# Optimization experiments

Measured on AMD Instinct MI355X. Metric: run time of the kernel, lower is better.

The kernel has to match this reference:

```python
import jax, jax.numpy as jnp
import numpy as np

EMB = 768
HEADS = 12
HEAD_DIM = EMB // HEADS
SCALE = HEAD_DIM ** -0.5


def setup_inputs() -> dict:
    key = jax.random.key(0)
    kq, kk, kv, kw = jax.random.split(key, 4)
    B, H, N, D = 2, HEADS, 2048, HEAD_DIM
    queries = jax.random.normal(kq, (B, H, N, D), dtype=jnp.float32)
    keys = jax.random.normal(kk, (B, H, N, D), dtype=jnp.float32)
    values = jax.random.normal(kv, (B, H, N, D), dtype=jnp.float32)
    proj_w = jax.random.normal(kw, (EMB, EMB), dtype=jnp.float32) * (EMB ** -0.5)
    proj_b = jnp.zeros((EMB,), dtype=jnp.float32)
    return {"queries": queries, "keys": keys, "values": values,
            "proj_w": proj_w, "proj_b": proj_b}


def reference(queries, keys, values, proj_w, proj_b):
    # energy: [b, h, n, n] -- full quadratic score matrix, as in the original
    energy = jnp.einsum('bhij,bhkj->bhik', queries, keys) * SCALE
    att = jax.nn.softmax(energy, axis=-1)  # att_drop_p=0.0 -> identity
    out = jnp.einsum('bhij,bhjk->bhik', att, values)  # [b, h, n, d]
    b, h, n, d = out.shape
    out = jnp.transpose(out, (0, 2, 1, 3)).reshape(b, n, h * d)  # 'b h n d -> b n (h d)'
    # nn.Linear: x @ W^T + b (projection dropout is inference identity)
    return out @ proj_w.T + proj_b
```

## Files before the change

### kernel.cpp

```cpp
#include <hip/hip_runtime.h>
#include <cstdint>

typedef short bf16x8 __attribute__((ext_vector_type(8)));
typedef float f32x4 __attribute__((ext_vector_type(4)));
typedef uint16_t u16x4 __attribute__((ext_vector_type(4)));

#define MFMA_16x16x32(a, b, c) __builtin_amdgcn_mfma_f32_16x16x32_bf16((a), (b), (c), 0, 0, 0)

static constexpr int BATCH = 2;
static constexpr int HEADS = 12;
static constexpr int NCTX  = 2048;
static constexpr int DH    = 64;
static constexpr int EMB   = 768;

static constexpr float QSCALE = 0.125f * 1.44269504088896340736f;

__device__ __forceinline__ uint16_t f2bf(float x) {
    uint32_t u = __float_as_uint(x);
    u += 0x7FFFu + ((u >> 16) & 1u);
    return (uint16_t)(u >> 16);
}
__device__ __forceinline__ uint32_t cvt_pk_bf16(float lo, float hi) {
    uint32_t r;
    asm("v_cvt_pk_bf16_f32 %0, %1, %2" : "=v"(r) : "v"(lo), "v"(hi));
    return r;
}

__global__ void k_cvt2(const float* __restrict__ a, uint16_t* __restrict__ da, int n4a,
                       const float* __restrict__ b2, uint16_t* __restrict__ db, int n4b) {
    int i = blockIdx.x * blockDim.x + threadIdx.x;
    const float* src; uint16_t* dst; int j;
    if (i < n4a) { src = a; dst = da; j = i; }
    else {
        j = i - n4a;
        if (j >= n4b) return;
        src = b2; dst = db;
    }
    float4 v = reinterpret_cast<const float4*>(src)[j];
    u16x4 hv = {f2bf(v.x), f2bf(v.y), f2bf(v.z), f2bf(v.w)};
    reinterpret_cast<u16x4*>(dst)[j] = hv;
}

__global__ __launch_bounds__(256) void k_vt(const float* __restrict__ v,
                                            uint16_t* __restrict__ vt) {
    const int bh = blockIdx.y;
    const int n0 = blockIdx.x * 64;
    const int t  = threadIdx.x;
    __shared__ uint16_t tileT[64][72];

    const int r  = t >> 2;
    const int cc = (t & 3) * 16;
    const float* vp = v + ((size_t)bh * NCTX + n0 + r) * DH + cc;
#pragma unroll
    for (int u = 0; u < 4; ++u) {
        float4 x = reinterpret_cast<const float4*>(vp)[u];
        tileT[cc + 4 * u + 0][r] = f2bf(x.x);
        tileT[cc + 4 * u + 1][r] = f2bf(x.y);
        tileT[cc + 4 * u + 2][r] = f2bf(x.z);
        tileT[cc + 4 * u + 3][r] = f2bf(x.w);
    }
    __syncthreads();

    const int l2 = t & 63;
    const int s0 = t >> 6;
    const int gg = l2 >> 4;
    const int c2 = l2 & 15;
    uint16_t* vb = vt + ((size_t)bh * 32 + (n0 >> 6)) * 8 * 512;
#pragma unroll
    for (int u = 0; u < 2; ++u) {
        const int slot = s0 + 4 * u;
        const int f = slot >> 1, h = slot & 1;
        bf16x8 x = *reinterpret_cast<const bf16x8*>(&tileT[f * 16 + c2][h * 32 + 8 * gg]);
        *reinterpret_cast<bf16x8*>(vb + (size_t)slot * 512 + l2 * 8) = x;
    }
}

__global__ __launch_bounds__(256) void k_attn(
        const float* __restrict__ q, const uint16_t* __restrict__ kb,
        const uint16_t* __restrict__ vf, uint16_t* __restrict__ xb) {
    const int bh = blockIdx.y;
    const int b  = bh / HEADS;
    const int h  = bh % HEADS;
    const int tid = threadIdx.x;
    const int w = tid >> 6;
    const int l = tid & 63;
    const int g = l >> 4;
    const int c = l & 15;

    __shared__ uint16_t K_s[2][64][72];
    __shared__ uint16_t P_s[4][16][72];

    const int q0 = blockIdx.x * 64 + w * 16;

    bf16x8 qa[2];
    {
        const float* qp = q + ((size_t)bh * NCTX + q0 + c) * DH + 8 * g;
#pragma unroll
        for (int kf = 0; kf < 2; ++kf) {
            float4 x0 = *reinterpret_cast<const float4*>(qp + kf * 32);
            float4 x1 = *reinterpret_cast<const float4*>(qp + kf * 32 + 4);
            bf16x8 f;
            f[0] = (short)f2bf(x0.x * QSCALE); f[1] = (short)f2bf(x0.y * QSCALE);
            f[2] = (short)f2bf(x0.z * QSCALE); f[3] = (short)f2bf(x0.w * QSCALE);
            f[4] = (short)f2bf(x1.x * QSCALE); f[5] = (short)f2bf(x1.y * QSCALE);
            f[6] = (short)f2bf(x1.z * QSCALE); f[7] = (short)f2bf(x1.w * QSCALE);
            qa[kf] = f;
        }
    }

    f32x4 zero = {0.f, 0.f, 0.f, 0.f};
    f32x4 o[4] = {zero, zero, zero, zero};
    float m = -1e30f;
    float lsum = 0.f;

    const int srow = tid >> 3;
    const int sch  = tid & 7;

    const uint16_t* kb_b = kb + (size_t)bh * NCTX * DH + srow * DH + sch * 8;
    const uint16_t* vf_b = vf + (size_t)bh * 32 * 8 * 512 + (size_t)l * 8;

    {
        bf16x8 a0 = *reinterpret_cast<const bf16x8*>(kb_b);
        bf16x8 a1 = *reinterpret_cast<const bf16x8*>(kb_b + 32 * DH);
        *reinterpret_cast<bf16x8*>(&K_s[0][srow][sch * 8])      = a0;
        *reinterpret_cast<bf16x8*>(&K_s[0][srow + 32][sch * 8]) = a1;
    }
    __syncthreads();

    for (int t = 0; t < NCTX / 64; ++t) {
        const int cur = t & 1;
        const int nxt = cur ^ 1;

        bf16x8 nk0, nk1;
        const bool pf = (t + 1) < NCTX / 64;
        if (pf) {
            const size_t ko = (size_t)(t + 1) * 64 * DH;
            nk0 = *reinterpret_cast<const bf16x8*>(kb_b + ko);
            nk1 = *reinterpret_cast<const bf16x8*>(kb_b + ko + 32 * DH);
        }

        bf16x8 vr[8];
#pragma unroll
        for (int s = 0; s < 8; ++s)
            vr[s] = *reinterpret_cast<const bf16x8*>(vf_b + ((size_t)t * 8 + s) * 512);

        f32x4 s[4] = {zero, zero, zero, zero};
        __builtin_amdgcn_s_setprio(1);
#pragma unroll
        for (int nf = 0; nf < 4; ++nf) {
#pragma unroll
            for (int kf = 0; kf < 2; ++kf) {
                bf16x8 bhf = *reinterpret_cast<const bf16x8*>(&K_s[cur][nf * 16 + c][kf * 32 + 8 * g]);
                s[nf] = MFMA_16x16x32(bhf, qa[kf], s[nf]);
            }
        }
        __builtin_amdgcn_s_setprio(0);

        float pm0 = fmaxf(fmaxf(s[0][0], s[0][1]), fmaxf(s[0][2], s[0][3]));
        float pm1 = fmaxf(fmaxf(s[1][0], s[1][1]), fmaxf(s[1][2], s[1][3]));
        float pm2 = fmaxf(fmaxf(s[2][0], s[2][1]), fmaxf(s[2][2], s[2][3]));
        float pm3 = fmaxf(fmaxf(s[3][0], s[3][1]), fmaxf(s[3][2], s[3][3]));
        float pmax = fmaxf(fmaxf(pm0, pm1), fmaxf(pm2, pm3));

        if (!__all(pmax <= m + 11.0f)) {
            float smax = fmaxf(pmax, __shfl_xor(pmax, 16));
            smax = fmaxf(smax, __shfl_xor(smax, 32));
            float mnew = fmaxf(m, smax);
            float corr = __builtin_amdgcn_exp2f(m - mnew);
            m = mnew;
            lsum *= corr;
#pragma unroll
            for (int r = 0; r < 4; ++r) {
                float cr = __shfl(corr, 4 * g + r);
#pragma unroll
                for (int f = 0; f < 4; ++f) o[f][r] *= cr;
            }
        }

#pragma unroll
        for (int nf = 0; nf < 4; ++nf) {
            float p0 = __builtin_amdgcn_exp2f(s[nf][0] - m);
            float p1 = __builtin_amdgcn_exp2f(s[nf][1] - m);
            float p2 = __builtin_amdgcn_exp2f(s[nf][2] - m);
            float p3 = __builtin_amdgcn_exp2f(s[nf][3] - m);
            lsum += (p0 + p1) + (p2 + p3);
            uint2 pk;
            pk.x = cvt_pk_bf16(p0, p1);
            pk.y = cvt_pk_bf16(p2, p3);
            *reinterpret_cast<uint2*>(&P_s[w][c][16 * nf + 4 * g]) = pk;
        }

        bf16x8 pa0 = *reinterpret_cast<const bf16x8*>(&P_s[w][c][8 * g]);
        bf16x8 pa1 = *reinterpret_cast<const bf16x8*>(&P_s[w][c][32 + 8 * g]);
        __builtin_amdgcn_s_setprio(1);
#pragma unroll
        for (int f = 0; f < 4; ++f) {
            o[f] = MFMA_16x16x32(pa0, vr[2 * f],     o[f]);
            o[f] = MFMA_16x16x32(pa1, vr[2 * f + 1], o[f]);
        }
        __builtin_amdgcn_s_setprio(0);

        if (pf) {
            *reinterpret_cast<bf16x8*>(&K_s[nxt][srow][sch * 8])      = nk0;
            *reinterpret_cast<bf16x8*>(&K_s[nxt][srow + 32][sch * 8]) = nk1;
        }
        __syncthreads();
    }

    lsum += __shfl_xor(lsum, 16);
    lsum += __shfl_xor(lsum, 32);
    const float linv = 1.0f / lsum;

    const size_t xbase = ((size_t)b * NCTX + q0) * EMB + h * DH;
#pragma unroll
    for (int r = 0; r < 4; ++r) {
        float lr = __shfl(linv, 4 * g + r);
#pragma unroll
        for (int f = 0; f < 4; ++f) {
            float v = o[f][r] * lr;
            size_t addr = xbase + (size_t)(4 * g + r) * EMB + f * 16 + c;
            xb[addr] = f2bf(v);
        }
    }
}

__global__ __launch_bounds__(256) void k_proj(
        const uint16_t* __restrict__ xb, const uint16_t* __restrict__ wb,
        const float* __restrict__ bias, float* __restrict__ out) {
    const int tid = threadIdx.x;
    const int w = tid >> 6;
    const int l = tid & 63;
    const int g = l >> 4;
    const int c = l & 15;
    const int m0 = blockIdx.x * 64 + w * 16;
    const int n0 = blockIdx.y * 64;

    __shared__ uint16_t W_s[64][72];

    f32x4 zero = {0.f, 0.f, 0.f, 0.f};
    f32x4 acc[4] = {zero, zero, zero, zero};

    const int srow = tid >> 2;
    const int sch  = tid & 3;
    constexpr int ROUNDS = EMB / 64;

    const uint16_t* whp = wb + (size_t)(n0 + srow) * EMB + sch * 8;
    const uint16_t* xhp = xb + (size_t)(m0 + c) * EMB + 8 * g;

    bf16x8 w0 = *reinterpret_cast<const bf16x8*>(whp);
    bf16x8 w1 = *reinterpret_cast<const bf16x8*>(whp + 32);
    bf16x8 a0 = *reinterpret_cast<const bf16x8*>(xhp);
    bf16x8 a1 = *reinterpret_cast<const bf16x8*>(xhp + 32);

    for (int rd = 0; rd < ROUNDS; ++rd) {
        __syncthreads();
        *reinterpret_cast<bf16x8*>(&W_s[srow][sch * 8])      = w0;
        *reinterpret_cast<bf16x8*>(&W_s[srow][32 + sch * 8]) = w1;
        __syncthreads();

        const int rn = (rd + 1 < ROUNDS) ? (rd + 1) : (ROUNDS - 1);
        bf16x8 w0n = *reinterpret_cast<const bf16x8*>(whp + (size_t)rn * 64);
        bf16x8 w1n = *reinterpret_cast<const bf16x8*>(whp + (size_t)rn * 64 + 32);
        bf16x8 a0n = *reinterpret_cast<const bf16x8*>(xhp + (size_t)rn * 64);
        bf16x8 a1n = *reinterpret_cast<const bf16x8*>(xhp + (size_t)rn * 64 + 32);

        __builtin_amdgcn_s_setprio(1);
#pragma unroll
        for (int nf = 0; nf < 4; ++nf) {
            bf16x8 b0 = *reinterpret_cast<const bf16x8*>(&W_s[nf * 16 + c][8 * g]);
            bf16x8 b1 = *reinterpret_cast<const bf16x8*>(&W_s[nf * 16 + c][32 + 8 * g]);
            acc[nf] = MFMA_16x16x32(a0, b0, acc[nf]);
            acc[nf] = MFMA_16x16x32(a1, b1, acc[nf]);
        }
        __builtin_amdgcn_s_setprio(0);

        w0 = w0n; w1 = w1n; a0 = a0n; a1 = a1n;
    }

#pragma unroll
    for (int nf = 0; nf < 4; ++nf) {
#pragma unroll
        for (int r = 0; r < 4; ++r) {
            int row = m0 + g * 4 + r;
            int col = n0 + nf * 16 + c;
            out[(size_t)row * EMB + col] = acc[nf][r] + bias[col];
        }
    }
}

extern "C" void kernel_launch(void* const* d_in, const int* in_sizes, int n_in,
                              void* d_out, int out_size, void* d_ws, size_t ws_size,
                              hipStream_t stream) {
    const float* q    = (const float*)d_in[0];
    const float* k    = (const float*)d_in[1];
    const float* v    = (const float*)d_in[2];
    const float* pw   = (const float*)d_in[3];
    const float* pb   = (const float*)d_in[4];
    float* out = (float*)d_out;

    const size_t nqkv = (size_t)BATCH * HEADS * NCTX * DH;
    const size_t nx   = (size_t)BATCH * NCTX * EMB;
    const size_t nw   = (size_t)EMB * EMB;

    uint8_t* ws = (uint8_t*)d_ws;
    uint16_t* kb = (uint16_t*)ws;              ws += nqkv * 2;
    uint16_t* vf = (uint16_t*)ws;              ws += nqkv * 2;
    uint16_t* xb = (uint16_t*)ws;              ws += nx * 2;
    uint16_t* wb = (uint16_t*)ws;              ws += nw * 2;

    const int n4k = (int)(nqkv / 4);
    const int n4w = (int)(nw / 4);
    k_cvt2<<<(n4k + n4w + 255) / 256, 256, 0, stream>>>(k, kb, n4k, pw, wb, n4w);
    k_vt<<<dim3(NCTX / 64, BATCH * HEADS), 256, 0, stream>>>(v, vf);

    k_attn<<<dim3(NCTX / 64, BATCH * HEADS), 256, 0, stream>>>(q, kb, vf, xb);

    k_proj<<<dim3((BATCH * NCTX) / 64, EMB / 64), 256, 0, stream>>>(xb, wb, pb, out);
}
```

Before: 77.59 us.

## Split attention KV range across two blocks and merge partial softmax results

Attention now runs a split-K style grid: each block processes half of the key/value sequence, and a new merge kernel combines the two partial outputs using their stored row max and sum. This doubles the block count from 768 to 1536, aiming for better occupancy and latency hiding across the GPU's compute units. It also drops the double-buffered K shared tile in favour of a single buffer with an extra barrier. In exchange it adds an extra kernel launch, writes and rereads bf16 partial outputs, and rounds to bf16 an extra time.

```diff
diff --git a/kernel.cpp b/kernel.cpp
--- a/kernel.cpp
+++ b/kernel.cpp
@@ -9,6 +9,7 @@
 
 static constexpr int BATCH = 2;
 static constexpr int HEADS = 12;
+static constexpr int BH    = BATCH * HEADS;
 static constexpr int NCTX  = 2048;
 static constexpr int DH    = 64;
 static constexpr int EMB   = 768;
@@ -19,6 +20,9 @@
     uint32_t u = __float_as_uint(x);
     u += 0x7FFFu + ((u >> 16) & 1u);
     return (uint16_t)(u >> 16);
+}
+__device__ __forceinline__ float bf2f(uint16_t h) {
+    return __uint_as_float(((uint32_t)h) << 16);
 }
 __device__ __forceinline__ uint32_t cvt_pk_bf16(float lo, float hi) {
     uint32_t r;
@@ -77,20 +81,21 @@
 
 __global__ __launch_bounds__(256) void k_attn(
         const float* __restrict__ q, const uint16_t* __restrict__ kb,
-        const uint16_t* __restrict__ vf, uint16_t* __restrict__ xb) {
+        const uint16_t* __restrict__ vf, uint16_t* __restrict__ of,
+        float* __restrict__ ml) {
     const int bh = blockIdx.y;
-    const int b  = bh / HEADS;
-    const int h  = bh % HEADS;
+    const int z  = blockIdx.z;
     const int tid = threadIdx.x;
     const int w = tid >> 6;
     const int l = tid & 63;
     const int g = l >> 4;
     const int c = l & 15;
 
-    __shared__ uint16_t K_s[2][64][72];
+    __shared__ uint16_t K_s[64][72];
     __shared__ uint16_t P_s[4][16][72];
 
     const int q0 = blockIdx.x * 64 + w * 16;
+    constexpr int NT = (NCTX / 2) / 64;
 
     bf16x8 qa[2];
     {
@@ -116,23 +121,20 @@
     const int srow = tid >> 3;
     const int sch  = tid & 7;
 
-    const uint16_t* kb_b = kb + (size_t)bh * NCTX * DH + srow * DH + sch * 8;
-    const uint16_t* vf_b = vf + (size_t)bh * 32 * 8 * 512 + (size_t)l * 8;
+    const uint16_t* kb_b = kb + ((size_t)bh * NCTX + z * (NCTX / 2) + srow) * DH + sch * 8;
+    const uint16_t* vf_b = vf + ((size_t)bh * 32 + z * NT) * 8 * 512 + (size_t)l * 8;
 
     {
         bf16x8 a0 = *reinterpret_cast<const bf16x8*>(kb_b);
         bf16x8 a1 = *reinterpret_cast<const bf16x8*>(kb_b + 32 * DH);
-        *reinterpret_cast<bf16x8*>(&K_s[0][srow][sch * 8])      = a0;
-        *reinterpret_cast<bf16x8*>(&K_s[0][srow + 32][sch * 8]) = a1;
+        *reinterpret_cast<bf16x8*>(&K_s[srow][sch * 8])      = a0;
+        *reinterpret_cast<bf16x8*>(&K_s[srow + 32][sch * 8]) = a1;
     }
     __syncthreads();
 
-    for (int t = 0; t < NCTX / 64; ++t) {
-        const int cur = t & 1;
-        const int nxt = cur ^ 1;
-
+    for (int t = 0; t < NT; ++t) {
         bf16x8 nk0, nk1;
-        const bool pf = (t + 1) < NCTX / 64;
+        const bool pf = (t + 1) < NT;
         if (pf) {
             const size_t ko = (size_t)(t + 1) * 64 * DH;
             nk0 = *reinterpret_cast<const bf16x8*>(kb_b + ko);
@@ -141,8 +143,8 @@
 
         bf16x8 vr[8];
 #pragma unroll
-        for (int s = 0; s < 8; ++s)
-            vr[s] = *reinterpret_cast<const bf16x8*>(vf_b + ((size_t)t * 8 + s) * 512);
+        for (int s2 = 0; s2 < 8; ++s2)
+            vr[s2] = *reinterpret_cast<const bf16x8*>(vf_b + ((size_t)t * 8 + s2) * 512);
 
         f32x4 s[4] = {zero, zero, zero, zero};
         __builtin_amdgcn_s_setprio(1);
@@ -150,7 +152,7 @@
         for (int nf = 0; nf < 4; ++nf) {
 #pragma unroll
             for (int kf = 0; kf < 2; ++kf) {
-                bf16x8 bhf = *reinterpret_cast<const bf16x8*>(&K_s[cur][nf * 16 + c][kf * 32 + 8 * g]);
+                bf16x8 bhf = *reinterpret_cast<const bf16x8*>(&K_s[nf * 16 + c][kf * 32 + 8 * g]);
                 s[nf] = MFMA_16x16x32(bhf, qa[kf], s[nf]);
             }
         }
@@ -200,9 +202,10 @@
         }
         __builtin_amdgcn_s_setprio(0);
 
+        __syncthreads();
         if (pf) {
-            *reinterpret_cast<bf16x8*>(&K_s[nxt][srow][sch * 8])      = nk0;
-            *reinterpret_cast<bf16x8*>(&K_s[nxt][srow + 32][sch * 8]) = nk1;
+            *reinterpret_cast<bf16x8*>(&K_s[srow][sch * 8])      = nk0;
+            *reinterpret_cast<bf16x8*>(&K_s[srow + 32][sch * 8]) = nk1;
         }
         __syncthreads();
     }
@@ -211,16 +214,52 @@
     lsum += __shfl_xor(lsum, 32);
     const float linv = 1.0f / lsum;
 
-    const size_t xbase = ((size_t)b * NCTX + q0) * EMB + h * DH;
+    const size_t obase = ((size_t)(z * BH + bh) * NCTX + q0) * DH;
 #pragma unroll
     for (int r = 0; r < 4; ++r) {
         float lr = __shfl(linv, 4 * g + r);
 #pragma unroll
         for (int f = 0; f < 4; ++f) {
             float v = o[f][r] * lr;
-            size_t addr = xbase + (size_t)(4 * g + r) * EMB + f * 16 + c;
-            xb[addr] = f2bf(v);
-        }
+            of[obase + (size_t)(4 * g + r) * DH + f * 16 + c] = f2bf(v);
+        }
+    }
+    if (l < 16) {
+        const size_t mli = 2 * ((size_t)(z * BH + bh) * NCTX + q0 + l);
+        ml[mli]     = m;
+        ml[mli + 1] = lsum;
+    }
+}
+
+__global__ __launch_bounds__(256) void k_mrg(const uint16_t* __restrict__ of,
+                                             const float* __restrict__ ml,
+                                             uint16_t* __restrict__ xb) {
+    const int row = blockIdx.x * 256 + threadIdx.x;
+    const int bh = row >> 11;
+    const int qq = row & (NCTX - 1);
+    const int b = bh / HEADS, h = bh % HEADS;
+    const size_t i0 = (size_t)bh * NCTX + qq;
+    const size_t i1 = (size_t)(BH + bh) * NCTX + qq;
+    const float m0 = ml[2 * i0], l0 = ml[2 * i0 + 1];
+    const float m1 = ml[2 * i1], l1 = ml[2 * i1 + 1];
+    const float M = fmaxf(m0, m1);
+    float c0 = l0 * __builtin_amdgcn_exp2f(m0 - M);
+    float c1 = l1 * __builtin_amdgcn_exp2f(m1 - M);
+    const float inv = 1.0f / (c0 + c1);
+    c0 *= inv; c1 *= inv;
+
+    const uint16_t* p0 = of + i0 * DH;
+    const uint16_t* p1 = of + i1 * DH;
+    uint16_t* xp = xb + ((size_t)b * NCTX + qq) * EMB + h * DH;
+#pragma unroll
+    for (int u = 0; u < 8; ++u) {
+        bf16x8 a  = *reinterpret_cast<const bf16x8*>(p0 + 8 * u);
+        bf16x8 bb = *reinterpret_cast<const bf16x8*>(p1 + 8 * u);
+        bf16x8 o8;
+#pragma unroll
+        for (int j = 0; j < 8; ++j)
+            o8[j] = (short)f2bf(bf2f((uint16_t)a[j]) * c0 + bf2f((uint16_t)bb[j]) * c1);
+        *reinterpret_cast<bf16x8*>(xp + 8 * u) = o8;
     }
 }
 
@@ -298,7 +337,7 @@
     const float* pb   = (const float*)d_in[4];
     float* out = (float*)d_out;
 
-    const size_t nqkv = (size_t)BATCH * HEADS * NCTX * DH;
+    const size_t nqkv = (size_t)BH * NCTX * DH;
     const size_t nx   = (size_t)BATCH * NCTX * EMB;
     const size_t nw   = (size_t)EMB * EMB;
 
@@ -307,13 +346,17 @@
     uint16_t* vf = (uint16_t*)ws;              ws += nqkv * 2;
     uint16_t* xb = (uint16_t*)ws;              ws += nx * 2;
     uint16_t* wb = (uint16_t*)ws;              ws += nw * 2;
+    uint16_t* of = (uint16_t*)ws;              ws += (size_t)2 * BH * NCTX * DH * 2;
+    float*    ml = (float*)ws;                 ws += (size_t)2 * BH * NCTX * 2 * 4;
 
     const int n4k = (int)(nqkv / 4);
     const int n4w = (int)(nw / 4);
     k_cvt2<<<(n4k + n4w + 255) / 256, 256, 0, stream>>>(k, kb, n4k, pw, wb, n4w);
-    k_vt<<<dim3(NCTX / 64, BATCH * HEADS), 256, 0, stream>>>(v, vf);
-
-    k_attn<<<dim3(NCTX / 64, BATCH * HEADS), 256, 0, stream>>>(q, kb, vf, xb);
+    k_vt<<<dim3(NCTX / 64, BH), 256, 0, stream>>>(v, vf);
+
+    k_attn<<<dim3(NCTX / 64, BH, 2), 256, 0, stream>>>(q, kb, vf, of, ml);
+
+    k_mrg<<<(BH * NCTX) / 256, 256, 0, stream>>>(of, ml, xb);
 
     k_proj<<<dim3((BATCH * NCTX) / 64, EMB / 64), 256, 0, stream>>>(xb, wb, pb, out);
 }
```

Result: slower. 86.43 us (+11.4%).

## Process 128 keys per attention iteration with single-buffered K tile

Applied to the files above, without the earlier changes.

The attention loop now handles 128 keys per iteration instead of 64, computing 8 score fragments at once and doing one online-softmax max update per 128 keys, then two P·V halves. The double-buffered 64-row K tile becomes a single 128-row buffer refilled between two barriers. The second half's V loads are issued after the QK MFMAs. This halves loop and barrier overhead per key but raises register pressure and adds an extra barrier per iteration, with no overlap of the K store into a second buffer.

```diff
diff --git a/kernel.cpp b/kernel.cpp
--- a/kernel.cpp
+++ b/kernel.cpp
@@ -9,6 +9,7 @@
 
 static constexpr int BATCH = 2;
 static constexpr int HEADS = 12;
+static constexpr int BH    = BATCH * HEADS;
 static constexpr int NCTX  = 2048;
 static constexpr int DH    = 64;
 static constexpr int EMB   = 768;
@@ -87,10 +88,11 @@
     const int g = l >> 4;
     const int c = l & 15;
 
-    __shared__ uint16_t K_s[2][64][72];
+    __shared__ uint16_t K_s[128][72];
     __shared__ uint16_t P_s[4][16][72];
 
     const int q0 = blockIdx.x * 64 + w * 16;
+    constexpr int NP = NCTX / 128;
 
     bf16x8 qa[2];
     {
@@ -116,51 +118,63 @@
     const int srow = tid >> 3;
     const int sch  = tid & 7;
 
-    const uint16_t* kb_b = kb + (size_t)bh * NCTX * DH + srow * DH + sch * 8;
+    const uint16_t* kb_b = kb + ((size_t)bh * NCTX + srow) * DH + sch * 8;
     const uint16_t* vf_b = vf + (size_t)bh * 32 * 8 * 512 + (size_t)l * 8;
 
-    {
-        bf16x8 a0 = *reinterpret_cast<const bf16x8*>(kb_b);
-        bf16x8 a1 = *reinterpret_cast<const bf16x8*>(kb_b + 32 * DH);
-        *reinterpret_cast<bf16x8*>(&K_s[0][srow][sch * 8])      = a0;
-        *reinterpret_cast<bf16x8*>(&K_s[0][srow + 32][sch * 8]) = a1;
+#pragma unroll
+    for (int u = 0; u < 4; ++u) {
+        bf16x8 a0 = *reinterpret_cast<const bf16x8*>(kb_b + (size_t)u * 32 * DH);
+        *reinterpret_cast<bf16x8*>(&K_s[srow + 32 * u][sch * 8]) = a0;
     }
     __syncthreads();
 
-    for (int t = 0; t < NCTX / 64; ++t) {
-        const int cur = t & 1;
-        const int nxt = cur ^ 1;
-
-        bf16x8 nk0, nk1;
-        const bool pf = (t + 1) < NCTX / 64;
+    for (int tp = 0; tp < NP; ++tp) {
+        bf16x8 nk[4];
+        const bool pf = (tp + 1) < NP;
         if (pf) {
-            const size_t ko = (size_t)(t + 1) * 64 * DH;
-            nk0 = *reinterpret_cast<const bf16x8*>(kb_b + ko);
-            nk1 = *reinterpret_cast<const bf16x8*>(kb_b + ko + 32 * DH);
-        }
-
-        bf16x8 vr[8];
-#pragma unroll
-        for (int s = 0; s < 8; ++s)
-            vr[s] = *reinterpret_cast<const bf16x8*>(vf_b + ((size_t)t * 8 + s) * 512);
-
-        f32x4 s[4] = {zero, zero, zero, zero};
+            const size_t ko = (size_t)(tp + 1) * 128 * DH;
+#pragma unroll
+            for (int u = 0; u < 4; ++u)
+                nk[u] = *reinterpret_cast<const bf16x8*>(kb_b + ko + (size_t)u * 32 * DH);
+        }
+
+        bf16x8 vra[8];
+#pragma unroll
+        for (int s2 = 0; s2 < 8; ++s2)
+            vra[s2] = *reinterpret_cast<const bf16x8*>(vf_b + ((size_t)(2 * tp) * 8 + s2) * 512);
+
+        f32x4 s[8];
+#pragma unroll
+        for (int nf = 0; nf < 8; ++nf) s[nf] = zero;
         __builtin_amdgcn_s_setprio(1);
 #pragma unroll
-        for (int nf = 0; nf < 4; ++nf) {
+        for (int nf = 0; nf < 8; ++nf) {
 #pragma unroll
             for (int kf = 0; kf < 2; ++kf) {
-                bf16x8 bhf = *reinterpret_cast<const bf16x8*>(&K_s[cur][nf * 16 + c][kf * 32 + 8 * g]);
+                bf16x8 bhf = *reinterpret_cast<const bf16x8*>(&K_s[nf * 16 + c][kf * 32 + 8 * g]);
                 s[nf] = MFMA_16x16x32(bhf, qa[kf], s[nf]);
             }
         }
         __builtin_amdgcn_s_setprio(0);
 
-        float pm0 = fmaxf(fmaxf(s[0][0], s[0][1]), fmaxf(s[0][2], s[0][3]));
-        float pm1 = fmaxf(fmaxf(s[1][0], s[1][1]), fmaxf(s[1][2], s[1][3]));
-        float pm2 = fmaxf(fmaxf(s[2][0], s[2][1]), fmaxf(s[2][2], s[2][3]));
-        float pm3 = fmaxf(fmaxf(s[3][0], s[3][1]), fmaxf(s[3][2], s[3][3]));
-        float pmax = fmaxf(fmaxf(pm0, pm1), fmaxf(pm2, pm3));
+        bf16x8 vrb[8];
+#pragma unroll
+        for (int s2 = 0; s2 < 8; ++s2)
+            vrb[s2] = *reinterpret_cast<const bf16x8*>(vf_b + ((size_t)(2 * tp + 1) * 8 + s2) * 512);
+
+        float pmax;
+        {
+            float t0 = fmaxf(fmaxf(s[0][0], s[0][1]), fmaxf(s[0][2], s[0][3]));
+            float t1 = fmaxf(fmaxf(s[1][0], s[1][1]), fmaxf(s[1][2], s[1][3]));
+            float t2 = fmaxf(fmaxf(s[2][0], s[2][1]), fmaxf(s[2][2], s[2][3]));
+            float t3 = fmaxf(fmaxf(s[3][0], s[3][1]), fmaxf(s[3][2], s[3][3]));
+            float t4 = fmaxf(fmaxf(s[4][0], s[4][1]), fmaxf(s[4][2], s[4][3]));
+            float t5 = fmaxf(fmaxf(s[5][0], s[5][1]), fmaxf(s[5][2], s[5][3]));
+            float t6 = fmaxf(fmaxf(s[6][0], s[6][1]), fmaxf(s[6][2], s[6][3]));
+            float t7 = fmaxf(fmaxf(s[7][0], s[7][1]), fmaxf(s[7][2], s[7][3]));
+            pmax = fmaxf(fmaxf(fmaxf(t0, t1), fmaxf(t2, t3)),
+                         fmaxf(fmaxf(t4, t5), fmaxf(t6, t7)));
+        }
 
         if (!__all(pmax <= m + 11.0f)) {
             float smax = fmaxf(pmax, __shfl_xor(pmax, 16));
@@ -189,20 +203,47 @@
             pk.y = cvt_pk_bf16(p2, p3);
             *reinterpret_cast<uint2*>(&P_s[w][c][16 * nf + 4 * g]) = pk;
         }
-
-        bf16x8 pa0 = *reinterpret_cast<const bf16x8*>(&P_s[w][c][8 * g]);
-        bf16x8 pa1 = *reinterpret_cast<const bf16x8*>(&P_s[w][c][32 + 8 * g]);
-        __builtin_amdgcn_s_setprio(1);
-#pragma unroll
-        for (int f = 0; f < 4; ++f) {
-            o[f] = MFMA_16x16x32(pa0, vr[2 * f],     o[f]);
-            o[f] = MFMA_16x16x32(pa1, vr[2 * f + 1], o[f]);
-        }
-        __builtin_amdgcn_s_setprio(0);
-
+        {
+            bf16x8 pa0 = *reinterpret_cast<const bf16x8*>(&P_s[w][c][8 * g]);
+            bf16x8 pa1 = *reinterpret_cast<const bf16x8*>(&P_s[w][c][32 + 8 * g]);
+            __builtin_amdgcn_s_setprio(1);
+#pragma unroll
+            for (int f = 0; f < 4; ++f) {
+                o[f] = MFMA_16x16x32(pa0, vra[2 * f],     o[f]);
+                o[f] = MFMA_16x16x32(pa1, vra[2 * f + 1], o[f]);
+            }
+            __builtin_amdgcn_s_setprio(0);
+        }
+
+#pragma unroll
+        for (int nf = 0; nf < 4; ++nf) {
+            float p0 = __builtin_amdgcn_exp2f(s[4 + nf][0] - m);
+            float p1 = __builtin_amdgcn_exp2f(s[4 + nf][1] - m);
+            float p2 = __builtin_amdgcn_exp2f(s[4 + nf][2] - m);
+            float p3 = __builtin_amdgcn_exp2f(s[4 + nf][3] - m);
+            lsum += (p0 + p1) + (p2 + p3);
+            uint2 pk;
+            pk.x = cvt_pk_bf16(p0, p1);
+            pk.y = cvt_pk_bf16(p2, p3);
+            *reinterpret_cast<uint2*>(&P_s[w][c][16 * nf + 4 * g]) = pk;
+        }
+        {
+            bf16x8 pa0 = *reinterpret_cast<const bf16x8*>(&P_s[w][c][8 * g]);
+            bf16x8 pa1 = *reinterpret_cast<const bf16x8*>(&P_s[w][c][32 + 8 * g]);
+            __builtin_amdgcn_s_setprio(1);
+#pragma unroll
+            for (int f = 0; f < 4; ++f) {
+                o[f] = MFMA_16x16x32(pa0, vrb[2 * f],     o[f]);
+                o[f] = MFMA_16x16x32(pa1, vrb[2 * f + 1], o[f]);
+            }
+            __builtin_amdgcn_s_setprio(0);
+        }
+
+        __syncthreads();
         if (pf) {
-            *reinterpret_cast<bf16x8*>(&K_s[nxt][srow][sch * 8])      = nk0;
-            *reinterpret_cast<bf16x8*>(&K_s[nxt][srow + 32][sch * 8]) = nk1;
+#pragma unroll
+            for (int u = 0; u < 4; ++u)
+                *reinterpret_cast<bf16x8*>(&K_s[srow + 32 * u][sch * 8]) = nk[u];
         }
         __syncthreads();
     }
@@ -298,7 +339,7 @@
     const float* pb   = (const float*)d_in[4];
     float* out = (float*)d_out;
 
-    const size_t nqkv = (size_t)BATCH * HEADS * NCTX * DH;
+    const size_t nqkv = (size_t)BH * NCTX * DH;
     const size_t nx   = (size_t)BATCH * NCTX * EMB;
     const size_t nw   = (size_t)EMB * EMB;
 
@@ -311,9 +352,9 @@
     const int n4k = (int)(nqkv / 4);
     const int n4w = (int)(nw / 4);
     k_cvt2<<<(n4k + n4w + 255) / 256, 256, 0, stream>>>(k, kb, n4k, pw, wb, n4w);
-    k_vt<<<dim3(NCTX / 64, BATCH * HEADS), 256, 0, stream>>>(v, vf);
-
-    k_attn<<<dim3(NCTX / 64, BATCH * HEADS), 256, 0, stream>>>(q, kb, vf, xb);
+    k_vt<<<dim3(NCTX / 64, BH), 256, 0, stream>>>(v, vf);
+
+    k_attn<<<dim3(NCTX / 64, BH), 256, 0, stream>>>(q, kb, vf, xb);
 
     k_proj<<<dim3((BATCH * NCTX) / 64, EMB / 64), 256, 0, stream>>>(xb, wb, pb, out);
 }
```

Result: slower. 87.90 us (+13.3%).
